# Kernel tuning notes

Measured on AMD Instinct MI355X. Metric: run time of the kernel, lower is better.

## Reference

```python
import jax, jax.numpy as jnp
import numpy as np

B, C, H, W = 32, 1536, 32, 32
M_CLUSTERS, L_DIM, G_DIM = 64, 128, 256
SINKHORN_ITERS = 3
EPS = 1e-12

def setup_inputs() -> dict:
    key = jax.random.key(0)
    ks = jax.random.split(key, 16)
    s = lambda i, shape, scale=0.02: jax.random.normal(ks[i], shape, jnp.float32) * scale
    return {
        'x': jax.random.normal(ks[0], (B, C, H, W), jnp.float32),
        't': jax.random.normal(ks[1], (B, C), jnp.float32),
        'cf_w1': s(2, (512, C)), 'cf_b1': s(3, (512,)),
        'cf_w2': s(4, (L_DIM, 512)), 'cf_b2': s(5, (L_DIM,)),
        'sc_w1': s(6, (512, C)), 'sc_b1': s(7, (512,)),
        'sc_w2': s(8, (M_CLUSTERS, 512)), 'sc_b2': s(9, (M_CLUSTERS,)),
        'tk_w1': s(10, (512, C)), 'tk_b1': s(11, (512,)),
        'tk_w2': s(12, (G_DIM, 512)), 'tk_b2': s(13, (G_DIM,)),
        'dust_bin': jnp.array(1.0, jnp.float32),
    }

def _l2norm(v, axis):
    n = jnp.sqrt(jnp.sum(v * v, axis=axis, keepdims=True))
    return v / jnp.maximum(n, EPS)

def _log_optimal_transport(scores, alpha, iters):
    # scores: [B, m, n]; append dustbin row, run log-space Sinkhorn
    b, m, n = scores.shape
    norm = -jnp.log(jnp.float32(m + n))
    bins = jnp.broadcast_to(alpha, (b, 1, n))
    Z0 = jnp.concatenate([scores, bins], axis=1)             # [B, m+1, n]
    log_mu = jnp.concatenate([jnp.full((m,), norm, jnp.float32),
                              jnp.log(jnp.float32(n - m))[None] + norm])  # [m+1]
    log_nu = jnp.full((n,), norm, jnp.float32)               # [n]
    u = jnp.zeros((b, m + 1), jnp.float32)
    v = jnp.zeros((b, n), jnp.float32)
    for _ in range(iters):
        u = log_mu[None, :] - jax.nn.logsumexp(Z0 + v[:, None, :], axis=2)
        v = log_nu[None, :] - jax.nn.logsumexp(Z0 + u[:, :, None], axis=1)
    return Z0 + u[:, :, None] + v[:, None, :] - norm

def reference(x, t, cf_w1, cf_b1, cf_w2, cf_b2, sc_w1, sc_b1, sc_w2, sc_b2,
              tk_w1, tk_b1, tk_w2, tk_b2, dust_bin):
    b = x.shape[0]
    xf = x.reshape(b, x.shape[1], -1)                        # [B, C, HW]
    # cluster_features: 1x1 conv stack -> [B, l, HW]
    h = jax.nn.relu(jnp.einsum('oc,bcn->bon', cf_w1, xf) + cf_b1[None, :, None])
    f = jnp.einsum('oc,bcn->bon', cf_w2, h) + cf_b2[None, :, None]
    # score: 1x1 conv stack -> [B, m, HW]
    h = jax.nn.relu(jnp.einsum('oc,bcn->bon', sc_w1, xf) + sc_b1[None, :, None])
    p = jnp.einsum('oc,bcn->bon', sc_w2, h) + sc_b2[None, :, None]
    # token_features: MLP -> [B, g]
    tk = jax.nn.relu(t @ tk_w1.T + tk_b1) @ tk_w2.T + tk_b2
    # Sinkhorn OT assignment, drop dustbin row
    p = jnp.exp(_log_optimal_transport(p, dust_bin, SINKHORN_ITERS))[:, :-1, :]  # [B, m, HW]
    # fused VLAD aggregation (avoids the repeat-materialized tensors)
    agg = jnp.einsum('bln,bmn->blm', f, p)                   # [B, l, m]
    agg = _l2norm(agg, axis=1).reshape(b, -1)                # [B, l*m]
    v = jnp.concatenate([_l2norm(tk, axis=-1), agg], axis=-1)
    return _l2norm(v, axis=-1)
```

## Files before the change

kernel.cpp:

```cpp
#include <hip/hip_runtime.h>
#include <hip/hip_bf16.h>
#include <math.h>

typedef unsigned short u16;
typedef __attribute__((ext_vector_type(8))) short short8;
typedef __attribute__((ext_vector_type(4))) float floatx4;

#define DEVINL __device__ __forceinline__

DEVINL float bf2f(u16 u) { union { unsigned int i; float f; } v; v.i = ((unsigned int)u) << 16; return v.f; }
DEVINL u16 f2bf(float f) {
  union { unsigned int i; float f; } v; v.f = f;
  unsigned int i = v.i;
  unsigned int r = (i + 0x7fffu + ((i >> 16) & 1u)) >> 16;
  return (u16)r;
}

__global__ __launch_bounds__(256) void k_prep(
    const float* __restrict__ cf_w1, u16* __restrict__ wc1,
    const float* __restrict__ sc_w1, u16* __restrict__ ws1,
    const float* __restrict__ cf_w2, u16* __restrict__ wc2,
    const float* __restrict__ sc_w2, u16* __restrict__ ws2p,
    const float* __restrict__ sc_b2, float* __restrict__ scb2p) {
  int i = blockIdx.x * 256 + threadIdx.x;
  int job = blockIdx.y;
  if (job == 4) {
    if (i < 128) scb2p[i] = (i < 64) ? sc_b2[i] : 0.f;
    return;
  }
  const float* src = (job == 0) ? cf_w1 : (job == 1) ? sc_w1 : (job == 2) ? cf_w2 : sc_w2;
  u16* dst = (job == 0) ? wc1 : (job == 1) ? ws1 : (job == 2) ? wc2 : ws2p;
  int n4 = (job <= 1) ? 196608 : 16384;
  if (i >= n4) return;
  ushort4 o = {0, 0, 0, 0};
  if (job != 3 || (i >> 7) < 64) {
    float4 v = ((const float4*)src)[i];
    o.x = f2bf(v.x); o.y = f2bf(v.y); o.z = f2bf(v.z); o.w = f2bf(v.w);
  }
  ((ushort4*)dst)[i] = o;
}

__global__ __launch_bounds__(256) void k_transpose(const float* __restrict__ x,
                                                   u16* __restrict__ xT,
                                                   int nC, int nN) {
  __shared__ u16 tile[64 * 65];
  int b = blockIdx.z;
  int c0 = blockIdx.y * 64, n0 = blockIdx.x * 64;
  const float* xb = x + ((long)b * nC + c0) * nN + n0;
  u16* xTb = xT + ((long)b * nN + n0) * nC + c0;
  int tid = threadIdx.x;
#pragma unroll
  for (int p = 0; p < 2; ++p) {
    int u = tid + p * 256;
    int r = u >> 3, nc = (u & 7) * 8;
    const float4* srcp = (const float4*)(xb + (long)r * nN + nc);
    float4 v0 = srcp[0], v1 = srcp[1];
    int base = r * 65 + nc;
    tile[base + 0] = f2bf(v0.x); tile[base + 1] = f2bf(v0.y);
    tile[base + 2] = f2bf(v0.z); tile[base + 3] = f2bf(v0.w);
    tile[base + 4] = f2bf(v1.x); tile[base + 5] = f2bf(v1.y);
    tile[base + 6] = f2bf(v1.z); tile[base + 7] = f2bf(v1.w);
  }
  __syncthreads();
#pragma unroll
  for (int p = 0; p < 2; ++p) {
    int u = tid + p * 256;
    int nr = u >> 3, cc = (u & 7) * 8;
    __align__(16) u16 tmp[8];
#pragma unroll
    for (int j = 0; j < 8; ++j) tmp[j] = tile[(cc + j) * 65 + nr];
    *(uint4*)(xTb + (long)nr * nC + cc) = *(uint4*)(tmp);
  }
}


#define K1_STAGE(S, H, SB)                                                     \
  if ((S) <= 23) {                                                             \
    const u16* gb_ = ((H) < 2) ? Bb : Ab;                                      \
    u16* lb_ = ((H) < 2) ? &Bs[SB][(H) & 1][0] : &As[SB][(H) & 1][0];          \
    int k0_ = (S) << 6;                                                        \
    _Pragma("unroll") for (int l_ = 0; l_ < 2; ++l_) {                         \
      int r_ = (wid * 2 + l_) * 8 + rIn;                                       \
      const u16* src_ =                                                        \
          gb_ + (long)(((H) & 1) * 128 + r_) * 1536 + k0_ + cSw;               \
      __builtin_amdgcn_global_load_lds(                                        \
          (const __attribute__((address_space(1))) void*)src_,                 \
          (__attribute__((address_space(3))) void*)(lb_ + (wid * 2 + l_) * 512), \
          16, 0, 0);                                                           \
    }                                                                          \
  }

#define K1_PHASE(P, SS, SH, SB, VMN)                                           \
  {                                                                            \
    short8 a00 = *(const short8*)(Aw + ((P)*2 + 0) * 1024 + aB0);              \
    short8 a01 = *(const short8*)(Aw + ((P)*2 + 0) * 1024 + aB1);              \
    short8 a10 = *(const short8*)(Aw + ((P)*2 + 1) * 1024 + aB0);              \
    short8 a11 = *(const short8*)(Aw + ((P)*2 + 1) * 1024 + aB1);              \
    if ((P) == 0) {                                                            \
      _Pragma("unroll") for (int n2 = 0; n2 < 4; ++n2) {                       \
        b[n2][0] = *(const short8*)(Bw + n2 * 1024 + aB0);                     \
        b[n2][1] = *(const short8*)(Bw + n2 * 1024 + aB1);                     \
      }                                                                        \
    }                                                                          \
    K1_STAGE(SS, SH, SB)                                                       \
    __builtin_amdgcn_s_barrier();                                              \
    asm volatile("s_waitcnt lgkmcnt(0)" ::: "memory");                         \
    __builtin_amdgcn_s_setprio(1);                                             \
    _Pragma("unroll") for (int n2 = 0; n2 < 4; ++n2) {                         \
      acc[(P)*2][n2] = __builtin_amdgcn_mfma_f32_16x16x32_bf16(                \
          a00, b[n2][0], acc[(P)*2][n2], 0, 0, 0);                             \
      acc[(P)*2][n2] = __builtin_amdgcn_mfma_f32_16x16x32_bf16(                \
          a01, b[n2][1], acc[(P)*2][n2], 0, 0, 0);                             \
      acc[(P)*2 + 1][n2] = __builtin_amdgcn_mfma_f32_16x16x32_bf16(            \
          a10, b[n2][0], acc[(P)*2 + 1][n2], 0, 0, 0);                         \
      acc[(P)*2 + 1][n2] = __builtin_amdgcn_mfma_f32_16x16x32_bf16(            \
          a11, b[n2][1], acc[(P)*2 + 1][n2], 0, 0, 0);                         \
    }                                                                          \
    __builtin_amdgcn_s_setprio(0);                                             \
    if ((VMN) == 6) {                                                          \
      asm volatile("s_waitcnt vmcnt(6)" ::: "memory");                         \
    } else if ((VMN) == 0) {                                                   \
      asm volatile("s_waitcnt vmcnt(0)" ::: "memory");                         \
    }                                                                          \
    __builtin_amdgcn_s_barrier();                                              \
  }

#define K1_TILE(T, BUF, VM)                                                    \
  {                                                                            \
    const u16* Aw = &As[BUF][wm][0];                                           \
    const u16* Bw = &Bs[BUF][wn >> 1][(wn & 1) * 4096];                        \
    short8 b[4][2];                                                            \
    K1_PHASE(0, (T) + 1, 3, (BUF) ^ 1, -1)                                     \
    K1_PHASE(1, (T) + 2, 0, (BUF), -1)                                         \
    K1_PHASE(2, (T) + 2, 1, (BUF), -1)                                         \
    K1_PHASE(3, (T) + 2, 2, (BUF), (VM))                                       \
  }

__global__ __launch_bounds__(512, 2) void k_gemm256(
    const u16* __restrict__ A,
    const u16* __restrict__ B1, const u16* __restrict__ B2,
    u16* __restrict__ Out,
    const float* __restrict__ bias1, const float* __restrict__ bias2) {
  __shared__ __align__(16) u16 As[2][2][8192];
  __shared__ __align__(16) u16 Bs[2][2][8192];
  int bz = blockIdx.z;
  int m0 = blockIdx.x * 256, n0 = blockIdx.y * 256;
  const u16* Ab = A + ((long)bz * 1024 + m0) * 1536;
  const u16* Bb = (n0 < 512) ? (B1 + (long)n0 * 1536)
                             : (B2 + (long)(n0 - 512) * 1536);
  int tid = threadIdx.x;
  int lane = tid & 63;
  int wid = tid >> 6;
  int wm = wid >> 2, wn = wid & 3;
  int lane16 = lane & 15, quad = lane >> 4;
  int rIn = lane >> 3;
  int cSw = ((lane & 7) ^ rIn) << 3;
  int aB0 = lane16 * 64 + ((quad ^ (lane16 & 7)) << 3);
  int aB1 = lane16 * 64 + (((4 + quad) ^ (lane16 & 7)) << 3);

  floatx4 acc[8][4];
#pragma unroll
  for (int i = 0; i < 8; ++i)
#pragma unroll
    for (int j = 0; j < 4; ++j) acc[i][j] = (floatx4){0.f, 0.f, 0.f, 0.f};

  K1_STAGE(0, 0, 0)
  K1_STAGE(0, 1, 0)
  K1_STAGE(0, 2, 0)
  K1_STAGE(0, 3, 0)
  K1_STAGE(1, 0, 1)
  K1_STAGE(1, 1, 1)
  K1_STAGE(1, 2, 1)
  asm volatile("s_waitcnt vmcnt(6)" ::: "memory");
  __builtin_amdgcn_s_barrier();

  for (int it = 0; it < 11; ++it) {
    K1_TILE(2 * it, 0, 6)
    K1_TILE(2 * it + 1, 1, 6)
  }
  K1_TILE(22, 0, 0)
  K1_TILE(23, 1, -1)

  const float* bcol = (n0 < 512) ? (bias1 + n0) : (bias2 + (n0 - 512));
  long obase = (long)bz * 1048576;
#pragma unroll
  for (int mi = 0; mi < 8; ++mi) {
    int row0 = m0 + wm * 128 + mi * 16 + quad * 4;
#pragma unroll
    for (int ni = 0; ni < 4; ++ni) {
      int colw = wn * 64 + ni * 16 + lane16;
      float bb = bcol[colw];
#pragma unroll
      for (int r = 0; r < 4; ++r) {
        float v = fmaxf(acc[mi][ni][r] + bb, 0.f);
        Out[obase + (long)(row0 + r) * 1024 + n0 + colw] = f2bf(v);
      }
    }
  }
}

__global__ __launch_bounds__(256) void k_k2dual(
    const u16* __restrict__ wA, const u16* __restrict__ wB,
    const u16* __restrict__ hT, u16* __restrict__ fOut, u16* __restrict__ sOut,
    const float* __restrict__ bA, const float* __restrict__ bB) {
  __shared__ __align__(16) u16 As[128 * 64];
  __shared__ __align__(16) u16 Bs[128 * 64];
  int sel = blockIdx.y, bz = blockIdx.z;
  const u16* A = sel ? wB : wA;
  const u16* Bbase = hT + (long)bz * 1048576 + (sel ? 512 : 0);
  u16* Out = (sel ? sOut : fOut) + (long)bz * 131072;
  const float* bias = sel ? bB : bA;
  int n0 = blockIdx.x * 128;
  int tid = threadIdx.x;
  int lane = tid & 63;
  int lane16 = lane & 15, quad = lane >> 4;
  int wid = tid >> 6;
  int wm = wid >> 1, wn = wid & 1;
  int rIn = lane >> 3;
  int kkSw = ((lane & 7) ^ rIn) * 8;

  floatx4 acc[4][4];
#pragma unroll
  for (int i = 0; i < 4; ++i)
#pragma unroll
    for (int j = 0; j < 4; ++j) acc[i][j] = (floatx4){0.f, 0.f, 0.f, 0.f};

  for (int k0 = 0; k0 < 512; k0 += 64) {
    __syncthreads();
#pragma unroll
    for (int h = 0; h < 4; ++h) {
      int ch = wid * 4 + h;
      int r = ch * 8 + rIn;
      const u16* srcA = A + (long)r * 512 + k0 + kkSw;
      __builtin_amdgcn_global_load_lds(
          (const __attribute__((address_space(1))) void*)srcA,
          (__attribute__((address_space(3))) void*)&As[ch * 512], 16, 0, 0);
      const u16* srcB = Bbase + (long)(n0 + r) * 1024 + k0 + kkSw;
      __builtin_amdgcn_global_load_lds(
          (const __attribute__((address_space(1))) void*)srcB,
          (__attribute__((address_space(3))) void*)&Bs[ch * 512], 16, 0, 0);
    }
    __syncthreads();
#pragma unroll
    for (int h2 = 0; h2 < 2; ++h2) {
      short8 af[4], bfr[4];
#pragma unroll
      for (int t = 0; t < 4; ++t) {
        int ra = wm * 64 + t * 16 + lane16;
        af[t] = *(const short8*)&As[ra * 64 + (((h2 * 4 + quad) ^ (ra & 7)) * 8)];
      }
#pragma unroll
      for (int t = 0; t < 4; ++t) {
        int rb = wn * 64 + t * 16 + lane16;
        bfr[t] = *(const short8*)&Bs[rb * 64 + (((h2 * 4 + quad) ^ (rb & 7)) * 8)];
      }
#pragma unroll
      for (int i = 0; i < 4; ++i)
#pragma unroll
        for (int j = 0; j < 4; ++j)
          acc[i][j] = __builtin_amdgcn_mfma_f32_16x16x32_bf16(af[i], bfr[j],
                                                              acc[i][j], 0, 0, 0);
    }
  }
#pragma unroll
  for (int i = 0; i < 4; ++i) {
    int rowb = wm * 64 + i * 16 + quad * 4;
#pragma unroll
    for (int j = 0; j < 4; ++j) {
      int col = n0 + wn * 64 + j * 16 + lane16;
#pragma unroll
      for (int r = 0; r < 4; ++r) {
        int row = rowb + r;
        Out[(long)row * 1024 + col] = f2bf(acc[i][j][r] + bias[row]);
      }
    }
  }
}

__global__ __launch_bounds__(1024) void k_sinkhorn(
    const u16* __restrict__ S, const float* __restrict__ alphaPtr,
    float lmu, float lmu_bin, float lnu, float norm, u16* __restrict__ P) {
  __shared__ float u_[65];
  __shared__ float v_[1024];
  int b = blockIdx.x, tid = threadIdx.x;
  const u16* Sb = S + (long)b * 131072;
  float alpha = *alphaPtr;
  v_[tid] = 0.f;
  __syncthreads();
  int wid = tid >> 6, lane = tid & 63;
  for (int it = 0; it < 3; ++it) {
    for (int i = wid; i < 65; i += 16) {
      float vals[16];
      float mx = -3.4e38f;
#pragma unroll
      for (int s = 0; s < 16; ++s) {
        int j = lane + s * 64;
        float z = (i < 64 ? bf2f(Sb[i * 1024 + j]) : alpha) + v_[j];
        vals[s] = z;
        mx = fmaxf(mx, z);
      }
#pragma unroll
      for (int off = 32; off > 0; off >>= 1) mx = fmaxf(mx, __shfl_xor(mx, off));
      float sum = 0.f;
#pragma unroll
      for (int s = 0; s < 16; ++s) sum += __expf(vals[s] - mx);
#pragma unroll
      for (int off = 32; off > 0; off >>= 1) sum += __shfl_xor(sum, off);
      if (lane == 0) u_[i] = (i < 64 ? lmu : lmu_bin) - (mx + __logf(sum));
    }
    __syncthreads();
    {
      float mx = alpha + u_[64];
#pragma unroll 8
      for (int i = 0; i < 64; ++i)
        mx = fmaxf(mx, bf2f(Sb[i * 1024 + tid]) + u_[i]);
      float sum = __expf(alpha + u_[64] - mx);
#pragma unroll 8
      for (int i = 0; i < 64; ++i)
        sum += __expf(bf2f(Sb[i * 1024 + tid]) + u_[i] - mx);
      v_[tid] = lnu - (mx + __logf(sum));
    }
    __syncthreads();
  }
  float vj = v_[tid];
  u16* Pb = P + (long)b * 65536;
#pragma unroll 8
  for (int i = 0; i < 64; ++i) {
    float z = bf2f(Sb[i * 1024 + tid]) + u_[i] + vj - norm;
    Pb[i * 1024 + tid] = f2bf(__expf(fminf(z, 1.0f)));
  }
}

__global__ __launch_bounds__(256) void k_agg(const u16* __restrict__ f,
                                             const u16* __restrict__ P,
                                             float* __restrict__ aggP) {
  __shared__ __align__(16) u16 Fs[128 * 32];
  __shared__ __align__(16) u16 Ps[64 * 32];
  int bz = blockIdx.z, kc = blockIdx.x;
  const u16* Fb = f + (long)bz * 128 * 1024;
  const u16* Pb = P + (long)bz * 64 * 1024;
  int tid = threadIdx.x, wid = tid >> 6, lane = tid & 63;
  int lane16 = lane & 15, quad = lane >> 4;
  int rA0 = lane >> 2, kk = (lane & 3) * 8;

  floatx4 acc[2][4];
#pragma unroll
  for (int i = 0; i < 2; ++i)
#pragma unroll
    for (int j = 0; j < 4; ++j) acc[i][j] = (floatx4){0.f, 0.f, 0.f, 0.f};

  for (int k0 = kc * 256; k0 < kc * 256 + 256; k0 += 32) {
    __syncthreads();
#pragma unroll
    for (int h = 0; h < 2; ++h) {
      int ch = wid * 2 + h;
      int r = ch * 16 + rA0;
      const u16* srcF = Fb + (long)r * 1024 + k0 + kk;
      __builtin_amdgcn_global_load_lds(
          (const __attribute__((address_space(1))) void*)srcF,
          (__attribute__((address_space(3))) void*)&Fs[ch * 512], 16, 0, 0);
    }
    {
      int r = wid * 16 + rA0;
      const u16* srcP = Pb + (long)r * 1024 + k0 + kk;
      __builtin_amdgcn_global_load_lds(
          (const __attribute__((address_space(1))) void*)srcP,
          (__attribute__((address_space(3))) void*)&Ps[wid * 512], 16, 0, 0);
    }
    __syncthreads();
    short8 af[2], bfr[4];
#pragma unroll
    for (int t = 0; t < 2; ++t)
      af[t] = *(const short8*)&Fs[(wid * 32 + t * 16 + lane16) * 32 + quad * 8];
#pragma unroll
    for (int j = 0; j < 4; ++j)
      bfr[j] = *(const short8*)&Ps[(j * 16 + lane16) * 32 + quad * 8];
#pragma unroll
    for (int i = 0; i < 2; ++i)
#pragma unroll
      for (int j = 0; j < 4; ++j)
        acc[i][j] = __builtin_amdgcn_mfma_f32_16x16x32_bf16(af[i], bfr[j],
                                                            acc[i][j], 0, 0, 0);
  }
  float* ab = aggP + ((long)kc * 32 + bz) * 8192;
#pragma unroll
  for (int i = 0; i < 2; ++i)
#pragma unroll
    for (int j = 0; j < 4; ++j)
#pragma unroll
      for (int r = 0; r < 4; ++r) {
        int row = wid * 32 + i * 16 + quad * 4 + r;
        int col = j * 16 + lane16;
        ab[row * 64 + col] = acc[i][j][r];
      }
}

DEVINL float waveSum(float x) {
#pragma unroll
  for (int off = 32; off > 0; off >>= 1) x += __shfl_xor(x, off);
  return x;
}

__global__ __launch_bounds__(256) void k_mlp1(const float* __restrict__ t,
                                              const float* __restrict__ w1,
                                              const float* __restrict__ b1,
                                              float* __restrict__ h1) {
  __shared__ float tl[1536];
  int b = blockIdx.y, og = blockIdx.x;
  int tid = threadIdx.x, wid = tid >> 6, lane = tid & 63;
  for (int i = tid; i < 1536; i += 256) tl[i] = t[b * 1536 + i];
  __syncthreads();
#pragma unroll 4
  for (int oi = 0; oi < 16; ++oi) {
    int o = og * 64 + wid * 16 + oi;
    const float* wr = w1 + (long)o * 1536;
    float acc = 0.f;
#pragma unroll
    for (int s = 0; s < 24; ++s) { int c = lane + s * 64; acc += tl[c] * wr[c]; }
    acc = waveSum(acc);
    if (lane == 0) h1[b * 512 + o] = fmaxf(acc + b1[o], 0.f);
  }
}

__global__ __launch_bounds__(256) void k_mlp2(const float* __restrict__ h1,
                                              const float* __restrict__ w2,
                                              const float* __restrict__ b2,
                                              float* __restrict__ tk) {
  __shared__ float hl[512];
  int b = blockIdx.y, og = blockIdx.x;
  int tid = threadIdx.x, wid = tid >> 6, lane = tid & 63;
  for (int i = tid; i < 512; i += 256) hl[i] = h1[b * 512 + i];
  __syncthreads();
#pragma unroll 4
  for (int oi = 0; oi < 16; ++oi) {
    int o = og * 64 + wid * 16 + oi;
    const float* wr = w2 + (long)o * 512;
    float acc = 0.f;
#pragma unroll
    for (int s = 0; s < 8; ++s) { int c = lane + s * 64; acc += hl[c] * wr[c]; }
    acc = waveSum(acc);
    if (lane == 0) tk[b * 256 + o] = acc + b2[o];
  }
}

DEVINL float blockSum256(float x, float* red) {
#pragma unroll
  for (int off = 32; off > 0; off >>= 1) x += __shfl_xor(x, off);
  int wid = threadIdx.x >> 6;
  __syncthreads();
  if ((threadIdx.x & 63) == 0) red[wid] = x;
  __syncthreads();
  return red[0] + red[1] + red[2] + red[3];
}

__global__ __launch_bounds__(256) void k_norms(const float* __restrict__ tk,
                                               const float* __restrict__ aggP,
                                               float* __restrict__ out) {
  __shared__ float asum[8192];
  __shared__ float cn[64];
  __shared__ float red[4];
  int b = blockIdx.x, tid = threadIdx.x;
  const float* a0 = aggP + (long)b * 8192;
  for (int idx = tid; idx < 8192; idx += 256)
    asum[idx] = a0[idx] + a0[32 * 8192 + idx] + a0[64 * 8192 + idx] +
                a0[96 * 8192 + idx];
  __syncthreads();
  float tkv = tk[b * 256 + tid];
  float tss = blockSum256(tkv * tkv, red);
  float tn = fmaxf(sqrtf(tss), 1e-12f);
  if (tid < 64) {
    float s = 0.f;
    for (int l = 0; l < 128; ++l) { float a = asum[l * 64 + tid]; s += a * a; }
    cn[tid] = fmaxf(sqrtf(s), 1e-12f);
  }
  __syncthreads();
  float gs = (tkv / tn) * (tkv / tn);
  for (int idx = tid; idx < 8192; idx += 256) {
    float a = asum[idx] / cn[idx & 63];
    gs += a * a;
  }
  float G = blockSum256(gs, red);
  float inv = 1.f / fmaxf(sqrtf(G), 1e-12f);
  float* ob = out + (long)b * 8448;
  ob[tid] = tkv / tn * inv;
  for (int idx = tid; idx < 8192; idx += 256)
    ob[256 + idx] = asum[idx] / cn[idx & 63] * inv;
}

extern "C" void kernel_launch(void* const* d_in, const int* in_sizes, int n_in,
                              void* d_out, int out_size, void* d_ws,
                              size_t ws_size, hipStream_t stream) {
  const float* x = (const float*)d_in[0];
  const float* t = (const float*)d_in[1];
  const float* cf_w1 = (const float*)d_in[2];
  const float* cf_b1 = (const float*)d_in[3];
  const float* cf_w2 = (const float*)d_in[4];
  const float* cf_b2 = (const float*)d_in[5];
  const float* sc_w1 = (const float*)d_in[6];
  const float* sc_b1 = (const float*)d_in[7];
  const float* sc_w2 = (const float*)d_in[8];
  const float* sc_b2 = (const float*)d_in[9];
  const float* tk_w1 = (const float*)d_in[10];
  const float* tk_b1 = (const float*)d_in[11];
  const float* tk_w2 = (const float*)d_in[12];
  const float* tk_b2 = (const float*)d_in[13];
  const float* dust = (const float*)d_in[14];
  float* out = (float*)d_out;

  char* ws = (char*)d_ws;
  size_t off = 0;
  u16* wc1 = (u16*)(ws + off); off += (size_t)512 * 1536 * 2;
  u16* ws1 = (u16*)(ws + off); off += (size_t)512 * 1536 * 2;
  u16* wc2 = (u16*)(ws + off); off += (size_t)128 * 512 * 2;
  u16* ws2p = (u16*)(ws + off); off += (size_t)128 * 512 * 2;
  float* scb2p = (float*)(ws + off); off += (size_t)128 * 4;
  u16* f = (u16*)(ws + off);   off += (size_t)32 * 128 * 1024 * 2;
  u16* scr = (u16*)(ws + off); off += (size_t)32 * 128 * 1024 * 2;
  u16* P = (u16*)(ws + off);   off += (size_t)32 * 64 * 1024 * 2;
  float* aggP = (float*)(ws + off); off += (size_t)4 * 32 * 128 * 64 * 4;
  float* h1ws = (float*)(ws + off); off += (size_t)32 * 512 * 4;
  float* tkws = (float*)(ws + off); off += (size_t)32 * 256 * 4;
  size_t fixed = off;
  size_t perB = (size_t)1024 * 1536 * 2 + (size_t)1024 * 1024 * 2;
  int c = 1;
  const int cands[6] = {32, 16, 8, 4, 2, 1};
  for (int k = 0; k < 6; ++k)
    if (fixed + (size_t)cands[k] * perB <= ws_size) { c = cands[k]; break; }
  u16* xT = (u16*)(ws + fixed);
  u16* hT = (u16*)(ws + fixed + (size_t)c * 1024 * 1536 * 2);

  k_prep<<<dim3(768, 5), 256, 0, stream>>>(cf_w1, wc1, sc_w1, ws1, cf_w2, wc2,
                                           sc_w2, ws2p, sc_b2, scb2p);

  k_mlp1<<<dim3(8, 32), 256, 0, stream>>>(t, tk_w1, tk_b1, h1ws);
  k_mlp2<<<dim3(4, 32), 256, 0, stream>>>(h1ws, tk_w2, tk_b2, tkws);

  float norm = -logf(1088.f);
  float lmu = norm;
  float lmu_bin = logf(960.f) + norm;
  float lnu = norm;

  for (int cb = 0; cb < 32; cb += c) {
    k_transpose<<<dim3(16, 24, c), 256, 0, stream>>>(
        x + (size_t)cb * 1536 * 1024, xT, 1536, 1024);
    k_gemm256<<<dim3(4, 4, c), 512, 0, stream>>>(xT, wc1, ws1, hT, cf_b1,
                                                 sc_b1);
    k_k2dual<<<dim3(8, 2, c), 256, 0, stream>>>(
        wc2, ws2p, hT, f + (size_t)cb * 131072, scr + (size_t)cb * 131072,
        cf_b2, scb2p);
  }
  k_sinkhorn<<<32, 1024, 0, stream>>>(scr, dust, lmu, lmu_bin, lnu, norm, P);
  k_agg<<<dim3(4, 1, 32), 256, 0, stream>>>(f, P, aggP);
  k_norms<<<32, 256, 0, stream>>>(tkws, aggP, out);
}
```

Baseline: 567.4 us.

## Fuse x transpose and bf16 conversion into the first GEMM's A-tile loads

Removes the separate transpose kernel and the xT workspace. The GEMM now reads fp32 x straight from global memory into registers, converts it to bf16 and writes it transposed and swizzled into LDS, with loads issued two stages ahead. This drops one full-size intermediate write and read of x, but adds register pressure and LDS-write work inside the GEMM main loop. Each GEMM block now re-reads fp32 x (twice the bytes of bf16) across its four N-blocks.

```diff
diff --git a/kernel.cpp b/kernel.cpp
--- a/kernel.cpp
+++ b/kernel.cpp
@@ -40,104 +40,123 @@
   ((ushort4*)dst)[i] = o;
 }
 
-__global__ __launch_bounds__(256) void k_transpose(const float* __restrict__ x,
-                                                   u16* __restrict__ xT,
-                                                   int nC, int nN) {
-  __shared__ u16 tile[64 * 65];
-  int b = blockIdx.z;
-  int c0 = blockIdx.y * 64, n0 = blockIdx.x * 64;
-  const float* xb = x + ((long)b * nC + c0) * nN + n0;
-  u16* xTb = xT + ((long)b * nN + n0) * nC + c0;
-  int tid = threadIdx.x;
-#pragma unroll
-  for (int p = 0; p < 2; ++p) {
-    int u = tid + p * 256;
-    int r = u >> 3, nc = (u & 7) * 8;
-    const float4* srcp = (const float4*)(xb + (long)r * nN + nc);
-    float4 v0 = srcp[0], v1 = srcp[1];
-    int base = r * 65 + nc;
-    tile[base + 0] = f2bf(v0.x); tile[base + 1] = f2bf(v0.y);
-    tile[base + 2] = f2bf(v0.z); tile[base + 3] = f2bf(v0.w);
-    tile[base + 4] = f2bf(v1.x); tile[base + 5] = f2bf(v1.y);
-    tile[base + 6] = f2bf(v1.z); tile[base + 7] = f2bf(v1.w);
-  }
-  __syncthreads();
-#pragma unroll
-  for (int p = 0; p < 2; ++p) {
-    int u = tid + p * 256;
-    int nr = u >> 3, cc = (u & 7) * 8;
-    __align__(16) u16 tmp[8];
-#pragma unroll
-    for (int j = 0; j < 8; ++j) tmp[j] = tile[(cc + j) * 65 + nr];
-    *(uint4*)(xTb + (long)nr * nC + cc) = *(uint4*)(tmp);
-  }
-}
-
-
-#define K1_STAGE(S, H, SB)                                                     \
+
+#define K1_AISSUE(S, H, AV)                                                    \
   if ((S) <= 23) {                                                             \
-    const u16* gb_ = ((H) < 2) ? Bb : Ab;                                      \
-    u16* lb_ = ((H) < 2) ? &Bs[SB][(H) & 1][0] : &As[SB][(H) & 1][0];          \
-    int k0_ = (S) << 6;                                                        \
+    const float* xp_ = Xb + (long)(((S) << 6) + kq) * 1024 + (H) * 128 + nbase;\
+    AV[0] = *(const float4*)(xp_);                                             \
+    AV[1] = *(const float4*)(xp_ + 1024);                                      \
+    AV[2] = *(const float4*)(xp_ + 2048);                                      \
+    AV[3] = *(const float4*)(xp_ + 3072);                                      \
+  }
+
+#define K1_AWRITE(S, DB)                                                       \
+  if ((S) <= 23) {                                                             \
+    _Pragma("unroll") for (int h_ = 0; h_ < 2; ++h_) {                         \
+      const float* fv_ = (const float*)(h_ ? avB : avA);                       \
+      u16* ah_ = &As[DB][h_][0];                                               \
+      _Pragma("unroll") for (int i_ = 0; i_ < 4; ++i_) {                       \
+        int row_ = nbase + i_;                                                 \
+        unsigned b0_ = f2bf(fv_[0 * 4 + i_]), b1_ = f2bf(fv_[4 + i_]);         \
+        unsigned b2_ = f2bf(fv_[8 + i_]), b3_ = f2bf(fv_[12 + i_]);            \
+        uint2 w_; w_.x = b0_ | (b1_ << 16); w_.y = b2_ | (b3_ << 16);          \
+        *(uint2*)&ah_[row_ * 64 + (((kq >> 3) ^ (row_ & 7)) << 3) + (kq & 4)] =\
+            w_;                                                                \
+      }                                                                        \
+    }                                                                          \
+  }
+
+#define K1_BSTAGE(S, H, SB)                                                    \
+  if ((S) <= 23) {                                                             \
     _Pragma("unroll") for (int l_ = 0; l_ < 2; ++l_) {                         \
-      int r_ = (wid * 2 + l_) * 8 + rIn;                                       \
-      const u16* src_ =                                                        \
-          gb_ + (long)(((H) & 1) * 128 + r_) * 1536 + k0_ + cSw;               \
+      int ch_ = wid * 2 + l_;                                                  \
+      int r_ = ch_ * 8 + rIn;                                                  \
+      const u16* src_ = Bb + (long)((H) * 128 + r_) * 1536 + ((S) << 6) + cSw; \
       __builtin_amdgcn_global_load_lds(                                        \
           (const __attribute__((address_space(1))) void*)src_,                 \
-          (__attribute__((address_space(3))) void*)(lb_ + (wid * 2 + l_) * 512), \
+          (__attribute__((address_space(3))) void*)(&Bs[SB][H][0] + ch_ * 512),\
           16, 0, 0);                                                           \
     }                                                                          \
   }
 
-#define K1_PHASE(P, SS, SH, SB, VMN)                                           \
+#define K1_READA(P)                                                            \
+  short8 a00 = *(const short8*)(Aw + ((P) * 2 + 0) * 1024 + aB0);              \
+  short8 a01 = *(const short8*)(Aw + ((P) * 2 + 0) * 1024 + aB1);              \
+  short8 a10 = *(const short8*)(Aw + ((P) * 2 + 1) * 1024 + aB0);              \
+  short8 a11 = *(const short8*)(Aw + ((P) * 2 + 1) * 1024 + aB1);
+
+#define K1_MFMAS(P)                                                            \
+  _Pragma("unroll") for (int n2 = 0; n2 < 4; ++n2) {                           \
+    acc[(P) * 2][n2] = __builtin_amdgcn_mfma_f32_16x16x32_bf16(                \
+        a00, b[n2][0], acc[(P) * 2][n2], 0, 0, 0);                             \
+    acc[(P) * 2][n2] = __builtin_amdgcn_mfma_f32_16x16x32_bf16(                \
+        a01, b[n2][1], acc[(P) * 2][n2], 0, 0, 0);                             \
+    acc[(P) * 2 + 1][n2] = __builtin_amdgcn_mfma_f32_16x16x32_bf16(            \
+        a10, b[n2][0], acc[(P) * 2 + 1][n2], 0, 0, 0);                         \
+    acc[(P) * 2 + 1][n2] = __builtin_amdgcn_mfma_f32_16x16x32_bf16(            \
+        a11, b[n2][1], acc[(P) * 2 + 1][n2], 0, 0, 0);                         \
+  }
+
+#define K1_TILE(T, BUF, VMN)                                                   \
   {                                                                            \
-    short8 a00 = *(const short8*)(Aw + ((P)*2 + 0) * 1024 + aB0);              \
-    short8 a01 = *(const short8*)(Aw + ((P)*2 + 0) * 1024 + aB1);              \
-    short8 a10 = *(const short8*)(Aw + ((P)*2 + 1) * 1024 + aB0);              \
-    short8 a11 = *(const short8*)(Aw + ((P)*2 + 1) * 1024 + aB1);              \
-    if ((P) == 0) {                                                            \
+    const u16* Aw = &As[BUF][wm][0];                                           \
+    const u16* Bw = &Bs[BUF][wn >> 1][0] + (wn & 1) * 4096;                    \
+    short8 b[4][2];                                                            \
+    {                                                             \
+      K1_READA(0)                                                              \
       _Pragma("unroll") for (int n2 = 0; n2 < 4; ++n2) {                       \
         b[n2][0] = *(const short8*)(Bw + n2 * 1024 + aB0);                     \
         b[n2][1] = *(const short8*)(Bw + n2 * 1024 + aB1);                     \
       }                                                                        \
+      if ((T) <= 22) { asm volatile("s_waitcnt vmcnt(4)" ::: "memory"); }      \
+      K1_AWRITE((T) + 1, (BUF) ^ 1)                                            \
+      K1_AISSUE((T) + 2, 0, avA)                                               \
+      __builtin_amdgcn_s_barrier();                                            \
+      asm volatile("s_waitcnt lgkmcnt(0)" ::: "memory");                       \
+      __builtin_amdgcn_s_setprio(1);                                           \
+      K1_MFMAS(0)                                                              \
+      __builtin_amdgcn_s_setprio(0);                                           \
+      __builtin_amdgcn_s_barrier();                                            \
     }                                                                          \
-    K1_STAGE(SS, SH, SB)                                                       \
-    __builtin_amdgcn_s_barrier();                                              \
-    asm volatile("s_waitcnt lgkmcnt(0)" ::: "memory");                         \
-    __builtin_amdgcn_s_setprio(1);                                             \
-    _Pragma("unroll") for (int n2 = 0; n2 < 4; ++n2) {                         \
-      acc[(P)*2][n2] = __builtin_amdgcn_mfma_f32_16x16x32_bf16(                \
-          a00, b[n2][0], acc[(P)*2][n2], 0, 0, 0);                             \
-      acc[(P)*2][n2] = __builtin_amdgcn_mfma_f32_16x16x32_bf16(                \
-          a01, b[n2][1], acc[(P)*2][n2], 0, 0, 0);                             \
-      acc[(P)*2 + 1][n2] = __builtin_amdgcn_mfma_f32_16x16x32_bf16(            \
-          a10, b[n2][0], acc[(P)*2 + 1][n2], 0, 0, 0);                         \
-      acc[(P)*2 + 1][n2] = __builtin_amdgcn_mfma_f32_16x16x32_bf16(            \
-          a11, b[n2][1], acc[(P)*2 + 1][n2], 0, 0, 0);                         \
+    {                                                             \
+      K1_READA(1)                                                              \
+      K1_AISSUE((T) + 2, 1, avB)                                               \
+      K1_BSTAGE((T) + 2, 0, (BUF))                                             \
+      __builtin_amdgcn_s_barrier();                                            \
+      asm volatile("s_waitcnt lgkmcnt(0)" ::: "memory");                       \
+      __builtin_amdgcn_s_setprio(1);                                           \
+      K1_MFMAS(1)                                                              \
+      __builtin_amdgcn_s_setprio(0);                                           \
+      __builtin_amdgcn_s_barrier();                                            \
     }                                                                          \
-    __builtin_amdgcn_s_setprio(0);                                             \
-    if ((VMN) == 6) {                                                          \
-      asm volatile("s_waitcnt vmcnt(6)" ::: "memory");                         \
-    } else if ((VMN) == 0) {                                                   \
-      asm volatile("s_waitcnt vmcnt(0)" ::: "memory");                         \
+    {                                                             \
+      K1_READA(2)                                                              \
+      K1_BSTAGE((T) + 2, 1, (BUF))                                             \
+      __builtin_amdgcn_s_barrier();                                            \
+      asm volatile("s_waitcnt lgkmcnt(0)" ::: "memory");                       \
+      __builtin_amdgcn_s_setprio(1);                                           \
+      K1_MFMAS(2)                                                              \
+      __builtin_amdgcn_s_setprio(0);                                           \
+      __builtin_amdgcn_s_barrier();                                            \
     }                                                                          \
-    __builtin_amdgcn_s_barrier();                                              \
-  }
-
-#define K1_TILE(T, BUF, VM)                                                    \
-  {                                                                            \
-    const u16* Aw = &As[BUF][wm][0];                                           \
-    const u16* Bw = &Bs[BUF][wn >> 1][(wn & 1) * 4096];                        \
-    short8 b[4][2];                                                            \
-    K1_PHASE(0, (T) + 1, 3, (BUF) ^ 1, -1)                                     \
-    K1_PHASE(1, (T) + 2, 0, (BUF), -1)                                         \
-    K1_PHASE(2, (T) + 2, 1, (BUF), -1)                                         \
-    K1_PHASE(3, (T) + 2, 2, (BUF), (VM))                                       \
+    {                                                             \
+      K1_READA(3)                                                              \
+      __builtin_amdgcn_s_barrier();                                            \
+      asm volatile("s_waitcnt lgkmcnt(0)" ::: "memory");                       \
+      __builtin_amdgcn_s_setprio(1);                                           \
+      K1_MFMAS(3)                                                              \
+      __builtin_amdgcn_s_setprio(0);                                           \
+      if ((VMN) == 12) {                                                       \
+        asm volatile("s_waitcnt vmcnt(12)" ::: "memory");                      \
+      } else if ((VMN) == 0) {                                                 \
+        asm volatile("s_waitcnt vmcnt(0)" ::: "memory");                       \
+      }                                                                        \
+      __builtin_amdgcn_s_barrier();                                            \
+    }                                                                          \
   }
 
 __global__ __launch_bounds__(512, 2) void k_gemm256(
-    const u16* __restrict__ A,
+    const float* __restrict__ X,
     const u16* __restrict__ B1, const u16* __restrict__ B2,
     u16* __restrict__ Out,
     const float* __restrict__ bias1, const float* __restrict__ bias2) {
@@ -145,7 +164,7 @@
   __shared__ __align__(16) u16 Bs[2][2][8192];
   int bz = blockIdx.z;
   int m0 = blockIdx.x * 256, n0 = blockIdx.y * 256;
-  const u16* Ab = A + ((long)bz * 1024 + m0) * 1536;
+  const float* Xb = X + (long)bz * 1536 * 1024 + m0;
   const u16* Bb = (n0 < 512) ? (B1 + (long)n0 * 1536)
                              : (B2 + (long)(n0 - 512) * 1536);
   int tid = threadIdx.x;
@@ -157,6 +176,9 @@
   int cSw = ((lane & 7) ^ rIn) << 3;
   int aB0 = lane16 * 64 + ((quad ^ (lane16 & 7)) << 3);
   int aB1 = lane16 * 64 + (((4 + quad) ^ (lane16 & 7)) << 3);
+  int kq = ((lane & 7) << 3) | (((lane >> 3) & 1) << 2);
+  int nbase = ((wid << 2) | (lane >> 4)) << 2;
+  float4 avA[4], avB[4];
 
   floatx4 acc[8][4];
 #pragma unroll
@@ -164,19 +186,23 @@
 #pragma unroll
     for (int j = 0; j < 4; ++j) acc[i][j] = (floatx4){0.f, 0.f, 0.f, 0.f};
 
-  K1_STAGE(0, 0, 0)
-  K1_STAGE(0, 1, 0)
-  K1_STAGE(0, 2, 0)
-  K1_STAGE(0, 3, 0)
-  K1_STAGE(1, 0, 1)
-  K1_STAGE(1, 1, 1)
-  K1_STAGE(1, 2, 1)
-  asm volatile("s_waitcnt vmcnt(6)" ::: "memory");
+  K1_AISSUE(0, 0, avA)
+  K1_AISSUE(0, 1, avB)
+  K1_BSTAGE(0, 0, 0)
+  K1_BSTAGE(0, 1, 0)
+  asm volatile("s_waitcnt vmcnt(4)" ::: "memory");
+  K1_AWRITE(0, 0)
+  K1_AISSUE(1, 0, avA)
+  K1_AISSUE(1, 1, avB)
+  K1_BSTAGE(1, 0, 1)
+  K1_BSTAGE(1, 1, 1)
+  asm volatile("s_waitcnt vmcnt(12)" ::: "memory");
+  asm volatile("s_waitcnt lgkmcnt(0)" ::: "memory");
   __builtin_amdgcn_s_barrier();
 
   for (int it = 0; it < 11; ++it) {
-    K1_TILE(2 * it, 0, 6)
-    K1_TILE(2 * it + 1, 1, 6)
+    K1_TILE(2 * it, 0, 12)
+    K1_TILE(2 * it + 1, 1, 12)
   }
   K1_TILE(22, 0, 0)
   K1_TILE(23, 1, -1)
@@ -521,13 +547,12 @@
   float* h1ws = (float*)(ws + off); off += (size_t)32 * 512 * 4;
   float* tkws = (float*)(ws + off); off += (size_t)32 * 256 * 4;
   size_t fixed = off;
-  size_t perB = (size_t)1024 * 1536 * 2 + (size_t)1024 * 1024 * 2;
+  size_t perB = (size_t)1024 * 1024 * 2;
   int c = 1;
   const int cands[6] = {32, 16, 8, 4, 2, 1};
   for (int k = 0; k < 6; ++k)
     if (fixed + (size_t)cands[k] * perB <= ws_size) { c = cands[k]; break; }
-  u16* xT = (u16*)(ws + fixed);
-  u16* hT = (u16*)(ws + fixed + (size_t)c * 1024 * 1536 * 2);
+  u16* hT = (u16*)(ws + fixed);
 
   k_prep<<<dim3(768, 5), 256, 0, stream>>>(cf_w1, wc1, sc_w1, ws1, cf_w2, wc2,
                                            sc_w2, ws2p, sc_b2, scb2p);
@@ -541,10 +566,8 @@
   float lnu = norm;
 
   for (int cb = 0; cb < 32; cb += c) {
-    k_transpose<<<dim3(16, 24, c), 256, 0, stream>>>(
-        x + (size_t)cb * 1536 * 1024, xT, 1536, 1024);
-    k_gemm256<<<dim3(4, 4, c), 512, 0, stream>>>(xT, wc1, ws1, hT, cf_b1,
-                                                 sc_b1);
+    k_gemm256<<<dim3(4, 4, c), 512, 0, stream>>>(
+        x + (size_t)cb * 1536 * 1024, wc1, ws1, hT, cf_b1, sc_b1);
     k_k2dual<<<dim3(8, 2, c), 256, 0, stream>>>(
         wc2, ws2p, hT, f + (size_t)cb * 131072, scr + (size_t)cb * 131072,
         cf_b2, scb2p);
```

Result: no change. 572.4 us (+0.9%).
